# Kernel optimization log

Hardware: AMD Instinct MI355X
Metric: run time of the kernel (lower is better)

## Reference

```python
import jax, jax.numpy as jnp
import numpy as np

D_H, D_MODEL, N_HEADS = 512, 2048, 8
HEAD_DIM = D_MODEL // N_HEADS
B, T = 4, 4096


def setup_inputs() -> dict:
    key = jax.random.key(0)
    ks = jax.random.split(key, 8)
    s_dm = 1.0 / np.sqrt(D_MODEL)
    s_dh = 1.0 / np.sqrt(D_H)
    return {
        "last_hidden": jax.random.normal(ks[0], (B, T, D_MODEL), dtype=jnp.float32),
        "zH": jax.random.normal(ks[1], (B, 1, D_H), dtype=jnp.float32),
        # weights stored as (in, out): y = x @ W  (equivalent to torch Linear with W.T)
        "W_mem": jax.random.normal(ks[2], (D_H, D_MODEL), dtype=jnp.float32) * s_dh,
        "W_q": jax.random.normal(ks[3], (D_MODEL, D_MODEL), dtype=jnp.float32) * s_dm,
        "W_k": jax.random.normal(ks[4], (D_MODEL, D_MODEL), dtype=jnp.float32) * s_dm,
        "W_v": jax.random.normal(ks[5], (D_MODEL, D_MODEL), dtype=jnp.float32) * s_dm,
        "W_o": jax.random.normal(ks[6], (D_MODEL, D_MODEL), dtype=jnp.float32) * s_dm,
        "gate": jnp.asarray(0.1, dtype=jnp.float32),
    }


def reference(last_hidden, zH, W_mem, W_q, W_k, W_v, W_o, gate):
    Bb, Tt, D = last_hidden.shape
    h, hd = N_HEADS, HEAD_DIM
    mem = zH @ W_mem                                   # (B, 1, D)
    Q = (last_hidden @ W_q).reshape(Bb, Tt, h, hd)     # (B, T, h, hd)
    K = (mem @ W_k).reshape(Bb, 1, h, hd)              # (B, 1, h, hd)
    V = (mem @ W_v).reshape(Bb, 1, h, hd)
    # att_logits: (B, h, T, 1); KV length is 1 so softmax -> ones (kept faithful)
    att_logits = jnp.einsum("bthd,bshd->bhts", Q, K) / np.sqrt(hd).astype(np.float32)
    att = jax.nn.softmax(att_logits, axis=-1)
    out = jnp.einsum("bhts,bshd->bthd", att, V).reshape(Bb, Tt, D)
    out = out @ W_o
    return last_hidden + jax.nn.sigmoid(gate) * out
```

## Files before the change

### kernel.cpp

```cpp
#include <hip/hip_runtime.h>
#include <hip/hip_bf16.h>

#define D_H     512
#define D_MODEL 2048
#define B_      4
#define T_      4096

__global__ void gemv_splitk(const float* __restrict__ x,
                            const float* __restrict__ W,
                            float* __restrict__ out,
                            int K, int N, int kchunk) {
    int j  = blockIdx.x * blockDim.x + threadIdx.x;
    int b  = blockIdx.y;
    int k0 = blockIdx.z * kchunk;
    extern __shared__ float xs[];
    for (int k = threadIdx.x; k < kchunk; k += blockDim.x)
        xs[k] = x[b * K + k0 + k];
    __syncthreads();
    if (j >= N) return;
    const float* Wp = W + (long)k0 * N + j;
    float acc = 0.f;
#pragma unroll 8
    for (int k = 0; k < kchunk; ++k)
        acc = fmaf(xs[k], Wp[(long)k * N], acc);
    atomicAdd(&out[b * N + j], acc);
}

__global__ void broadcast_add(const float4* __restrict__ lh,
                              const float* __restrict__ r,
                              const float* __restrict__ gate,
                              float4* __restrict__ out) {
    const long CHUNKS = (long)B_ * T_ * D_MODEL / 4;
    long i = (long)blockIdx.x * blockDim.x + threadIdx.x;
    if (i >= CHUNKS) return;

    float g = gate[0];
    float s = 1.0f / (1.0f + __expf(-g));

    long e0 = i * 4;
    int  b  = (int)(e0 >> 23);
    int  d  = (int)(e0 & (D_MODEL - 1));

    float4 rv = *reinterpret_cast<const float4*>(r + b * D_MODEL + d);
    float4 v  = lh[i];

    float4 o;
    o.x = fmaf(s, rv.x, v.x);
    o.y = fmaf(s, rv.y, v.y);
    o.z = fmaf(s, rv.z, v.z);
    o.w = fmaf(s, rv.w, v.w);
    out[i] = o;
}

extern "C" void kernel_launch(void* const* d_in, const int* in_sizes, int n_in,
                              void* d_out, int out_size, void* d_ws, size_t ws_size,
                              hipStream_t stream) {
    const float* lh    = (const float*)d_in[0];
    const float* zH    = (const float*)d_in[1];
    const float* W_mem = (const float*)d_in[2];
    const float* W_v   = (const float*)d_in[5];
    const float* W_o   = (const float*)d_in[6];
    const float* gate  = (const float*)d_in[7];
    float* out = (float*)d_out;

    float* mem = (float*)d_ws;
    float* V   = mem + B_ * D_MODEL;
    float* r   = V   + B_ * D_MODEL;
    hipMemsetAsync(d_ws, 0, (size_t)3 * B_ * D_MODEL * sizeof(float), stream);

    dim3 blk(256);

    {
        dim3 grd(D_MODEL / 256, B_, 8);
        gemv_splitk<<<grd, blk, 64 * sizeof(float), stream>>>(
            zH, W_mem, mem, D_H, D_MODEL, 64);
    }
    {
        dim3 grd(D_MODEL / 256, B_, 8);
        gemv_splitk<<<grd, blk, 256 * sizeof(float), stream>>>(
            mem, W_v, V, D_MODEL, D_MODEL, 256);
    }
    {
        dim3 grd(D_MODEL / 256, B_, 8);
        gemv_splitk<<<grd, blk, 256 * sizeof(float), stream>>>(
            V, W_o, r, D_MODEL, D_MODEL, 256);
    }
    {
        long chunks = (long)B_ * T_ * D_MODEL / 4;
        dim3 grd((unsigned)((chunks + 255) / 256));
        broadcast_add<<<grd, blk, 0, stream>>>(
            (const float4*)lh, r, gate, (float4*)out);
    }
}
```

Before: 310.2 us.

## Batch all four rows per GEMV weight load and use nontemporal streaming

The split-K GEMV now processes all four batch rows in one thread, so each weight element is loaded once and used four times instead of being reloaded per batch. K-chunks are made template constants with smaller chunks and more splits. The broadcast-add uses nontemporal loads and stores for the large streaming tensor and drops the bounds check. More atomics per block and exact-divisibility assumptions are the trade-offs.

```diff
diff --git a/kernel.cpp b/kernel.cpp
--- a/kernel.cpp
+++ b/kernel.cpp
@@ -6,33 +6,45 @@
 #define B_      4
 #define T_      4096
 
-__global__ void gemv_splitk(const float* __restrict__ x,
-                            const float* __restrict__ W,
-                            float* __restrict__ out,
-                            int K, int N, int kchunk) {
-    int j  = blockIdx.x * blockDim.x + threadIdx.x;
-    int b  = blockIdx.y;
-    int k0 = blockIdx.z * kchunk;
-    extern __shared__ float xs[];
-    for (int k = threadIdx.x; k < kchunk; k += blockDim.x)
-        xs[k] = x[b * K + k0 + k];
+typedef float vfloat4 __attribute__((ext_vector_type(4)));
+
+template <int KCHUNK>
+__global__ void gemv4_splitk(const float* __restrict__ x,
+                             const float* __restrict__ W,
+                             float* __restrict__ out,
+                             int K, int N) {
+    __shared__ float xs[4][KCHUNK];
+    const int tid = threadIdx.x;
+    const int j   = blockIdx.x * blockDim.x + tid;
+    const int k0  = blockIdx.y * KCHUNK;
+
+    for (int i = tid; i < 4 * KCHUNK; i += blockDim.x) {
+        int b = i / KCHUNK, k = i - b * KCHUNK;
+        xs[b][k] = x[b * K + k0 + k];
+    }
     __syncthreads();
-    if (j >= N) return;
+
+    float a0 = 0.f, a1 = 0.f, a2 = 0.f, a3 = 0.f;
     const float* Wp = W + (long)k0 * N + j;
-    float acc = 0.f;
 #pragma unroll 8
-    for (int k = 0; k < kchunk; ++k)
-        acc = fmaf(xs[k], Wp[(long)k * N], acc);
-    atomicAdd(&out[b * N + j], acc);
+    for (int k = 0; k < KCHUNK; ++k) {
+        float w = Wp[(long)k * N];
+        a0 = fmaf(xs[0][k], w, a0);
+        a1 = fmaf(xs[1][k], w, a1);
+        a2 = fmaf(xs[2][k], w, a2);
+        a3 = fmaf(xs[3][k], w, a3);
+    }
+    atomicAdd(&out[0 * N + j], a0);
+    atomicAdd(&out[1 * N + j], a1);
+    atomicAdd(&out[2 * N + j], a2);
+    atomicAdd(&out[3 * N + j], a3);
 }
 
-__global__ void broadcast_add(const float4* __restrict__ lh,
+__global__ void broadcast_add(const vfloat4* __restrict__ lh,
                               const float* __restrict__ r,
                               const float* __restrict__ gate,
-                              float4* __restrict__ out) {
-    const long CHUNKS = (long)B_ * T_ * D_MODEL / 4;
+                              vfloat4* __restrict__ out) {
     long i = (long)blockIdx.x * blockDim.x + threadIdx.x;
-    if (i >= CHUNKS) return;
 
     float g = gate[0];
     float s = 1.0f / (1.0f + __expf(-g));
@@ -41,15 +53,15 @@
     int  b  = (int)(e0 >> 23);
     int  d  = (int)(e0 & (D_MODEL - 1));
 
-    float4 rv = *reinterpret_cast<const float4*>(r + b * D_MODEL + d);
-    float4 v  = lh[i];
+    vfloat4 rv = *reinterpret_cast<const vfloat4*>(r + b * D_MODEL + d);
+    vfloat4 v  = __builtin_nontemporal_load(lh + i);
 
-    float4 o;
+    vfloat4 o;
     o.x = fmaf(s, rv.x, v.x);
     o.y = fmaf(s, rv.y, v.y);
     o.z = fmaf(s, rv.z, v.z);
     o.w = fmaf(s, rv.w, v.w);
-    out[i] = o;
+    __builtin_nontemporal_store(o, out + i);
 }
 
 extern "C" void kernel_launch(void* const* d_in, const int* in_sizes, int n_in,
@@ -66,29 +78,26 @@
     float* mem = (float*)d_ws;
     float* V   = mem + B_ * D_MODEL;
     float* r   = V   + B_ * D_MODEL;
-    hipMemsetAsync(d_ws, 0, (size_t)3 * B_ * D_MODEL * sizeof(float), stream);
+    (void)hipMemsetAsync(d_ws, 0, (size_t)3 * B_ * D_MODEL * sizeof(float), stream);
 
     dim3 blk(256);
 
     {
-        dim3 grd(D_MODEL / 256, B_, 8);
-        gemv_splitk<<<grd, blk, 64 * sizeof(float), stream>>>(
-            zH, W_mem, mem, D_H, D_MODEL, 64);
+        dim3 grd(D_MODEL / 256, 32);
+        gemv4_splitk<16><<<grd, blk, 0, stream>>>(zH, W_mem, mem, D_H, D_MODEL);
     }
     {
-        dim3 grd(D_MODEL / 256, B_, 8);
-        gemv_splitk<<<grd, blk, 256 * sizeof(float), stream>>>(
-            mem, W_v, V, D_MODEL, D_MODEL, 256);
+        dim3 grd(D_MODEL / 256, 32);
+        gemv4_splitk<64><<<grd, blk, 0, stream>>>(mem, W_v, V, D_MODEL, D_MODEL);
     }
     {
-        dim3 grd(D_MODEL / 256, B_, 8);
-        gemv_splitk<<<grd, blk, 256 * sizeof(float), stream>>>(
-            V, W_o, r, D_MODEL, D_MODEL, 256);
+        dim3 grd(D_MODEL / 256, 32);
+        gemv4_splitk<64><<<grd, blk, 0, stream>>>(V, W_o, r, D_MODEL, D_MODEL);
     }
     {
         long chunks = (long)B_ * T_ * D_MODEL / 4;
-        dim3 grd((unsigned)((chunks + 255) / 256));
+        dim3 grd((unsigned)(chunks / 256));
         broadcast_add<<<grd, blk, 0, stream>>>(
-            (const float4*)lh, r, gate, (float4*)out);
+            (const vfloat4*)lh, r, gate, (vfloat4*)out);
     }
 }
```

Measured after the change: 282.1 us. 9.1% less time.
